# Optimization experiments

Measured on AMD Instinct MI355X. Metric: run time of the kernel, lower is better.

Reference implementation:

```python
import jax, jax.numpy as jnp
import numpy as np

N, D, H, E, K = 4096, 512, 2048, 8, 2  # tokens, input_size, hidden_size, num_experts, top_k


def setup_inputs() -> dict:
    key = jax.random.key(0)
    ks = jax.random.split(key, 4)
    x = jax.random.normal(ks[0], (N, D), dtype=jnp.float32)
    # torch init: weights ~ N(0, 0.001), biases zero
    Wg = jax.random.normal(ks[1], (D, E), dtype=jnp.float32) * 0.001
    bg = jnp.zeros((E,), jnp.float32)
    W1 = jax.random.normal(ks[2], (E, D, H), dtype=jnp.float32) * 0.001
    b1 = jnp.zeros((E, H), jnp.float32)
    W2 = jax.random.normal(ks[3], (E, H, D), dtype=jnp.float32) * 0.001
    b2 = jnp.zeros((E, D), jnp.float32)
    return {"x": x, "Wg": Wg, "bg": bg, "W1": W1, "b1": b1, "W2": W2, "b2": b2}


def reference(x, Wg, bg, W1, b1, W2, b2):
    # Gating: softmax over experts
    gates = jax.nn.softmax(x @ Wg + bg, axis=-1)            # [N, E]
    top_w, top_i = jax.lax.top_k(gates, K)                  # [N, K]
    top_w = top_w / jnp.sum(top_w, axis=-1, keepdims=True)  # renormalize

    # Expert MLP (fc1 -> fc2, no nonlinearity per source). Vectorized across all
    # experts, then gather the top-k selected outputs per token.
    h1 = jnp.einsum('nd,edh->neh', x, W1) + b1              # [N, E, H]
    all_out = jnp.einsum('neh,ehd->ned', h1, W2) + b2       # [N, E, D]
    sel = jnp.take_along_axis(all_out, top_i[:, :, None], axis=1)  # [N, K, D]

    combined = jnp.einsum('nkd,nk->nd', sel, top_w)         # [N, D]

    # usage counts: scatter-add of (detached) top-k weights per expert
    usage = jnp.zeros((E,), x.dtype).at[top_i.reshape(-1)].add(
        jax.lax.stop_gradient(top_w).reshape(-1))
    return combined, usage
```

## Files before the change

### kernel.cpp

```cpp
#include <hip/hip_runtime.h>
#include <hip/hip_bf16.h>


#define N_TOK 4096
#define DIM   512
#define HID   2048
#define NEXP  8
#define TOTSLOT (2 * N_TOK)
#define M1TILE 72
#define M2TILE 144

typedef __attribute__((ext_vector_type(8))) short short8;
typedef __attribute__((ext_vector_type(4))) float f32x4;

static __device__ __forceinline__ unsigned short f2bf(float f) {
    __hip_bfloat16 b = __float2bfloat16(f);
    return *reinterpret_cast<unsigned short*>(&b);
}
static __device__ __forceinline__ float bf2f(unsigned short u) {
    return __uint_as_float((unsigned)u << 16);
}

static __device__ __forceinline__ void load16_to_lds(const void* g, void* l) {
    __builtin_amdgcn_global_load_lds(
        (const __attribute__((address_space(1))) unsigned int*)g,
        (__attribute__((address_space(3))) unsigned int*)l, 16, 0, 0);
}

__global__ __launch_bounds__(256) void gating_kernel(
    const float* __restrict__ x, const float* __restrict__ Wg,
    const float* __restrict__ bg,
    int* __restrict__ cnt, int* __restrict__ te, float* __restrict__ tw,
    float* __restrict__ usage, unsigned short* __restrict__ Xb)
{
    __shared__ int   lcnt[NEXP];
    __shared__ float lus[NEXP];
    int tid = threadIdx.x;
    if (tid < NEXP) { lcnt[tid] = 0; lus[tid] = 0.f; }
    __syncthreads();

    int wave = tid >> 6;
    int lane = tid & 63;

    for (int t = 0; t < 4; ++t) {
        int n = blockIdx.x * 16 + wave * 4 + t;

        float acc[NEXP];
#pragma unroll
        for (int e = 0; e < NEXP; ++e) acc[e] = 0.f;

#pragma unroll
        for (int it = 0; it < DIM / 64; ++it) {
            int d = it * 64 + lane;
            float xv = x[n * DIM + d];
            Xb[n * DIM + d] = f2bf(xv);
            float4 wa = *(const float4*)&Wg[d * NEXP];
            float4 wb = *(const float4*)&Wg[d * NEXP + 4];
            acc[0] += xv * wa.x; acc[1] += xv * wa.y;
            acc[2] += xv * wa.z; acc[3] += xv * wa.w;
            acc[4] += xv * wb.x; acc[5] += xv * wb.y;
            acc[6] += xv * wb.z; acc[7] += xv * wb.w;
        }
#pragma unroll
        for (int m = 32; m >= 1; m >>= 1) {
#pragma unroll
            for (int e = 0; e < NEXP; ++e)
                acc[e] += __shfl_xor(acc[e], m, 64);
        }
        if (lane == 0) {
            float l[NEXP];
#pragma unroll
            for (int e = 0; e < NEXP; ++e) l[e] = acc[e] + bg[e];
            int i0 = 0;
#pragma unroll
            for (int e = 1; e < NEXP; ++e) if (l[e] > l[i0]) i0 = e;
            int i1 = (i0 == 0) ? 1 : 0;
#pragma unroll
            for (int e = 0; e < NEXP; ++e)
                if (e != i0 && l[e] > l[i1]) i1 = e;
            float w0 = 1.f / (1.f + expf(l[i1] - l[i0]));
            float w1 = 1.f - w0;
            te[n * 2] = i0; te[n * 2 + 1] = i1;
            tw[n * 2] = w0; tw[n * 2 + 1] = w1;
            atomicAdd(&lcnt[i0], 1);
            atomicAdd(&lcnt[i1], 1);
            atomicAdd(&lus[i0], w0);
            atomicAdd(&lus[i1], w1);
        }
    }
    __syncthreads();
    if (tid < NEXP) {
        if (lcnt[tid]) atomicAdd(&cnt[tid], lcnt[tid]);
        if (lus[tid] != 0.f) atomicAdd(&usage[tid], lus[tid]);
    }
}

__global__ void prefix_kernel(const int* __restrict__ cnt,
                              int* __restrict__ offs, int* __restrict__ fill,
                              int* __restrict__ tb128, int* __restrict__ tb64,
                              int* __restrict__ ntile)
{
    if (threadIdx.x == 0) {
        int s = 0, a = 0, b = 0;
        for (int e = 0; e < NEXP; ++e) {
            offs[e] = s; s += cnt[e];
            tb128[e] = a; a += (cnt[e] + 127) >> 7;
            tb64[e]  = b; b += (cnt[e] + 63) >> 6;
        }
        tb128[NEXP] = a; tb64[NEXP] = b;
        ntile[0] = a; ntile[1] = b;
    }
    if (threadIdx.x < NEXP) fill[threadIdx.x] = 0;
}

__global__ __launch_bounds__(256) void scatter_kernel(
    int* __restrict__ te, const float* __restrict__ tw,
    const int* __restrict__ offs, int* __restrict__ fill,
    int* __restrict__ btok, float* __restrict__ bwt)
{
    __shared__ int lcnt[NEXP];
    __shared__ int gbase[NEXP];
    int tid = threadIdx.x;
    if (tid < NEXP) lcnt[tid] = 0;
    __syncthreads();
    int n = blockIdx.x * 256 + tid;
    int e0 = te[n * 2], e1 = te[n * 2 + 1];
    int l0 = atomicAdd(&lcnt[e0], 1);
    int l1 = atomicAdd(&lcnt[e1], 1);
    __syncthreads();
    if (tid < NEXP) gbase[tid] = atomicAdd(&fill[tid], lcnt[tid]);
    __syncthreads();
    int s0 = offs[e0] + gbase[e0] + l0;
    int s1 = offs[e1] + gbase[e1] + l1;
    btok[s0] = n; bwt[s0] = tw[n * 2];
    btok[s1] = n; bwt[s1] = tw[n * 2 + 1];
    te[n * 2] = s0; te[n * 2 + 1] = s1;
}

__global__ __launch_bounds__(256) void transpose_cvt_kernel(
    const float* __restrict__ W1, const float* __restrict__ W2,
    unsigned short* __restrict__ W1t, unsigned short* __restrict__ W2t,
    int* __restrict__ cnt, float* __restrict__ usage)
{
    __shared__ unsigned short tile[64][65];
    int tid = threadIdx.x;
    int bx = blockIdx.x, z = blockIdx.y;
    if (bx == 0 && z == 0 && tid < NEXP) { cnt[tid] = 0; usage[tid] = 0.f; }

    const float* in; unsigned short* outp; int R, C, rt, ct, e;
    if (z < NEXP) { e = z;        in = W1; outp = W1t; R = DIM; C = HID; rt = bx >> 5; ct = bx & 31; }
    else          { e = z - NEXP; in = W2; outp = W2t; R = HID; C = DIM; rt = bx >> 3; ct = bx & 7;  }
    const float* src = in + (size_t)e * R * C;
    unsigned short* dst = outp + (size_t)e * R * C;
    int r0 = rt * 64, c0 = ct * 64;
    int rr = tid >> 2, cb = (tid & 3) * 16;
#pragma unroll
    for (int i = 0; i < 4; ++i) {
        float4 v = *(const float4*)&src[(size_t)(r0 + rr) * C + c0 + cb + i * 4];
        tile[rr][cb + i * 4 + 0] = f2bf(v.x);
        tile[rr][cb + i * 4 + 1] = f2bf(v.y);
        tile[rr][cb + i * 4 + 2] = f2bf(v.z);
        tile[rr][cb + i * 4 + 3] = f2bf(v.w);
    }
    __syncthreads();
#pragma unroll
    for (int i = 0; i < 4; ++i) {
        ushort4 u;
        u.x = tile[cb + i * 4 + 0][rr];
        u.y = tile[cb + i * 4 + 1][rr];
        u.z = tile[cb + i * 4 + 2][rr];
        u.w = tile[cb + i * 4 + 3][rr];
        *(ushort4*)&dst[(size_t)(c0 + rr) * R + r0 + cb + i * 4] = u;
    }
}


__global__ __launch_bounds__(256) void gemm1_kernel(
    const unsigned short* __restrict__ Xb, const unsigned short* __restrict__ W1t,
    const float* __restrict__ b1, const int* __restrict__ cnt,
    const int* __restrict__ offs, const int* __restrict__ btok,
    const int* __restrict__ tb128, const int* __restrict__ ntile,
    unsigned short* __restrict__ H1)
{
    __shared__ __align__(16) unsigned short Ws[2][128 * 64];
    __shared__ __align__(16) unsigned short Xs[2][128 * 64];
    __shared__ int tok_s[128];

    int bx = blockIdx.x;
    int ti = (bx & 7) * (M1TILE / 8) + (bx >> 3);
    if (ti >= ntile[0]) return;
    int e = 0;
#pragma unroll
    for (int k = 1; k < NEXP; ++k) if (ti >= tb128[k]) e = k;
    int tt = ti - tb128[e];
    int ht = blockIdx.y;
    int cn = cnt[e];
    int off_e = offs[e];
    int tid = threadIdx.x;

    if (tid < 128) {
        int lr = tt * 128 + tid;
        tok_s[tid] = (lr < cn) ? btok[off_e + lr] : 0;
    }
    __syncthreads();

    int wave = tid >> 6, lane = tid & 63;
    int mbase = (wave >> 1) * 64, nbase = (wave & 1) * 64;
    int quad = lane >> 4, lcol = lane & 15;
    f32x4 acc[4][4];
#pragma unroll
    for (int mi = 0; mi < 4; ++mi)
#pragma unroll
        for (int ni = 0; ni < 4; ++ni)
            acc[mi][ni] = (f32x4){0.f, 0.f, 0.f, 0.f};

    int Rb = tid >> 3, pc = tid & 7;
    const unsigned short* Wsrc = W1t + ((size_t)e * HID + ht * 128) * DIM;

    auto stage = [&](int buf, int k0) {
#pragma unroll
        for (int p = 0; p < 4; ++p) {
            int R = Rb + p * 32;
            int c = pc ^ (R & 7);
            load16_to_lds(&Wsrc[(size_t)R * DIM + k0 + c * 8], &Ws[buf][R * 64 + pc * 8]);
            load16_to_lds(&Xb[(size_t)tok_s[R] * DIM + k0 + c * 8], &Xs[buf][R * 64 + pc * 8]);
        }
    };

    stage(0, 0);

    const int NT = DIM / 64;
    for (int t = 0; t < NT; ++t) {
        int cur = t & 1;
        if (t + 1 < NT) {
            stage(cur ^ 1, (t + 1) * 64);
            asm volatile("s_waitcnt vmcnt(8)" ::: "memory");
        } else {
            asm volatile("s_waitcnt vmcnt(0)" ::: "memory");
        }
        __builtin_amdgcn_s_barrier();
        __builtin_amdgcn_sched_barrier(0);
#pragma unroll
        for (int h = 0; h < 2; ++h) {
            int cs = ((h * 4 + quad) ^ (lcol & 7)) * 8;
            short8 a[4], b[4];
#pragma unroll
            for (int i = 0; i < 4; ++i) {
                a[i] = *(const short8*)&Ws[cur][(mbase + i * 16 + lcol) * 64 + cs];
                b[i] = *(const short8*)&Xs[cur][(nbase + i * 16 + lcol) * 64 + cs];
            }
#pragma unroll
            for (int mi = 0; mi < 4; ++mi)
#pragma unroll
                for (int ni = 0; ni < 4; ++ni)
                    acc[mi][ni] = __builtin_amdgcn_mfma_f32_16x16x32_bf16(
                        a[mi], b[ni], acc[mi][ni], 0, 0, 0);
        }
        __builtin_amdgcn_sched_barrier(0);
        __builtin_amdgcn_s_barrier();
    }

    float4 bv[4];
#pragma unroll
    for (int mi = 0; mi < 4; ++mi)
        bv[mi] = *(const float4*)&b1[e * HID + ht * 128 + mbase + mi * 16 + quad * 4];
#pragma unroll
    for (int ni = 0; ni < 4; ++ni) {
        int tn = tt * 128 + nbase + ni * 16 + lcol;
        if (tn >= cn) continue;
        size_t srow = (size_t)(off_e + tn) * HID + ht * 128;
#pragma unroll
        for (int mi = 0; mi < 4; ++mi) {
            int hh = mbase + mi * 16 + quad * 4;
            ushort4 u;
            u.x = f2bf(acc[mi][ni][0] + bv[mi].x);
            u.y = f2bf(acc[mi][ni][1] + bv[mi].y);
            u.z = f2bf(acc[mi][ni][2] + bv[mi].z);
            u.w = f2bf(acc[mi][ni][3] + bv[mi].w);
            *(ushort4*)&H1[srow + hh] = u;
        }
    }
}

__global__ __launch_bounds__(256) void gemm2_kernel(
    const unsigned short* __restrict__ H1, const unsigned short* __restrict__ W2t,
    const float* __restrict__ b2, const int* __restrict__ cnt,
    const int* __restrict__ offs, const float* __restrict__ bwt,
    const int* __restrict__ tb64, const int* __restrict__ ntile,
    unsigned short* __restrict__ O)
{
    __shared__ __align__(16) unsigned short Ws[2][128 * 64];
    __shared__ __align__(16) unsigned short Hs[2][64 * 64];
    __shared__ float wt_s[64];

    int bx = blockIdx.x;
    int ti = (bx & 7) * (M2TILE / 8) + (bx >> 3);
    if (ti >= ntile[1]) return;
    int e = 0;
#pragma unroll
    for (int k = 1; k < NEXP; ++k) if (ti >= tb64[k]) e = k;
    int tt = ti - tb64[e];
    int dt = blockIdx.y;
    int cn = cnt[e];
    int off_e = offs[e];
    int sb = off_e + tt * 64;
    int tid = threadIdx.x;

    if (tid < 64) {
        int lr = tt * 64 + tid;
        wt_s[tid] = (lr < cn) ? bwt[off_e + lr] : 0.f;
    }

    int wave = tid >> 6, lane = tid & 63;
    int nbase = wave * 32;
    int quad = lane >> 4, lcol = lane & 15;
    f32x4 acc[4][2];
#pragma unroll
    for (int mi = 0; mi < 4; ++mi)
#pragma unroll
        for (int ni = 0; ni < 2; ++ni)
            acc[mi][ni] = (f32x4){0.f, 0.f, 0.f, 0.f};

    int Rb = tid >> 3, pc = tid & 7;
    const unsigned short* Wsrc = W2t + ((size_t)e * DIM + dt * 128) * HID;

    auto stage = [&](int buf, int k0) {
#pragma unroll
        for (int p = 0; p < 4; ++p) {
            int R = Rb + p * 32;
            int c = pc ^ (R & 7);
            load16_to_lds(&Wsrc[(size_t)R * HID + k0 + c * 8], &Ws[buf][R * 64 + pc * 8]);
        }
#pragma unroll
        for (int p = 0; p < 2; ++p) {
            int R = Rb + p * 32;
            int c = pc ^ (R & 7);
            int sr = sb + R; if (sr > TOTSLOT - 1) sr = TOTSLOT - 1;
            load16_to_lds(&H1[(size_t)sr * HID + k0 + c * 8], &Hs[buf][R * 64 + pc * 8]);
        }
    };

    stage(0, 0);

    const int NT = HID / 64;
    for (int t = 0; t < NT; ++t) {
        int cur = t & 1;
        if (t + 1 < NT) {
            stage(cur ^ 1, (t + 1) * 64);
            asm volatile("s_waitcnt vmcnt(6)" ::: "memory");
        } else {
            asm volatile("s_waitcnt vmcnt(0)" ::: "memory");
        }
        __builtin_amdgcn_s_barrier();
        __builtin_amdgcn_sched_barrier(0);
#pragma unroll
        for (int h = 0; h < 2; ++h) {
            int cs = ((h * 4 + quad) ^ (lcol & 7)) * 8;
            short8 a[4], b[2];
#pragma unroll
            for (int i = 0; i < 4; ++i)
                a[i] = *(const short8*)&Hs[cur][(i * 16 + lcol) * 64 + cs];
#pragma unroll
            for (int i = 0; i < 2; ++i)
                b[i] = *(const short8*)&Ws[cur][(nbase + i * 16 + lcol) * 64 + cs];
#pragma unroll
            for (int mi = 0; mi < 4; ++mi)
#pragma unroll
                for (int ni = 0; ni < 2; ++ni)
                    acc[mi][ni] = __builtin_amdgcn_mfma_f32_16x16x32_bf16(
                        a[mi], b[ni], acc[mi][ni], 0, 0, 0);
        }
        __builtin_amdgcn_sched_barrier(0);
        __builtin_amdgcn_s_barrier();
    }

    unsigned short* Oe = O + (size_t)sb * DIM + dt * 128;
#pragma unroll
    for (int ni = 0; ni < 2; ++ni) {
        int dl = nbase + ni * 16 + lcol;
        float bv = b2[e * DIM + dt * 128 + dl];
#pragma unroll
        for (int mi = 0; mi < 4; ++mi) {
            int rl = mi * 16 + quad * 4;
#pragma unroll
            for (int r = 0; r < 4; ++r) {
                int sl = rl + r;
                if (tt * 64 + sl < cn)
                    Oe[(size_t)sl * DIM + dl] = f2bf(wt_s[sl] * (acc[mi][ni][r] + bv));
            }
        }
    }
}

__global__ __launch_bounds__(256) void combine_kernel(
    const unsigned short* __restrict__ O, const int* __restrict__ sidx,
    float* __restrict__ out)
{
    int tid = threadIdx.x;
    int n = blockIdx.x * 2 + (tid >> 7);
    int dd = (tid & 127) * 4;
    int s0 = sidx[n * 2], s1 = sidx[n * 2 + 1];
    ushort4 a = *(const ushort4*)&O[(size_t)s0 * DIM + dd];
    ushort4 c = *(const ushort4*)&O[(size_t)s1 * DIM + dd];
    float4 o;
    o.x = bf2f(a.x) + bf2f(c.x);
    o.y = bf2f(a.y) + bf2f(c.y);
    o.z = bf2f(a.z) + bf2f(c.z);
    o.w = bf2f(a.w) + bf2f(c.w);
    *(float4*)&out[(size_t)n * DIM + dd] = o;
}

#define TN 16
#define HC 256
#define NCHUNK (HID / HC)

__global__ __launch_bounds__(256) void gating_fb_kernel(
    const float* __restrict__ x, const float* __restrict__ Wg,
    const float* __restrict__ bg,
    int* __restrict__ cnt, int* __restrict__ btok, float* __restrict__ bwt,
    float* __restrict__ usage)
{
    int wave = threadIdx.x >> 6;
    int lane = threadIdx.x & 63;
    int n = blockIdx.x * 4 + wave;
    float acc[NEXP];
#pragma unroll
    for (int e = 0; e < NEXP; ++e) acc[e] = 0.f;
    for (int d = lane; d < DIM; d += 64) {
        float xv = x[n * DIM + d];
        float4 wa = *(const float4*)&Wg[d * NEXP];
        float4 wb = *(const float4*)&Wg[d * NEXP + 4];
        acc[0] += xv * wa.x; acc[1] += xv * wa.y;
        acc[2] += xv * wa.z; acc[3] += xv * wa.w;
        acc[4] += xv * wb.x; acc[5] += xv * wb.y;
        acc[6] += xv * wb.z; acc[7] += xv * wb.w;
    }
#pragma unroll
    for (int m = 32; m >= 1; m >>= 1)
#pragma unroll
        for (int e = 0; e < NEXP; ++e)
            acc[e] += __shfl_xor(acc[e], m, 64);
    if (lane == 0) {
        float l[NEXP];
#pragma unroll
        for (int e = 0; e < NEXP; ++e) l[e] = acc[e] + bg[e];
        int i0 = 0;
#pragma unroll
        for (int e = 1; e < NEXP; ++e) if (l[e] > l[i0]) i0 = e;
        int i1 = (i0 == 0) ? 1 : 0;
#pragma unroll
        for (int e = 0; e < NEXP; ++e)
            if (e != i0 && l[e] > l[i1]) i1 = e;
        float w0 = 1.f / (1.f + expf(l[i1] - l[i0]));
        float w1 = 1.f - w0;
        int p0 = atomicAdd(&cnt[i0], 1);
        btok[i0 * N_TOK + p0] = n; bwt[i0 * N_TOK + p0] = w0;
        int p1 = atomicAdd(&cnt[i1], 1);
        btok[i1 * N_TOK + p1] = n; bwt[i1 * N_TOK + p1] = w1;
        atomicAdd(&usage[i0], w0);
        atomicAdd(&usage[i1], w1);
    }
}

__global__ __launch_bounds__(256) void expert_fb_kernel(
    const float* __restrict__ x, const float* __restrict__ W1,
    const float* __restrict__ b1, const float* __restrict__ W2,
    const float* __restrict__ b2, const int* __restrict__ cnt,
    const int* __restrict__ btok, const float* __restrict__ bwt,
    float* __restrict__ out)
{
    __shared__ float xs[TN][DIM];
    __shared__ float h1s[TN][HC];
    __shared__ int   tok_s[TN];
    __shared__ float wt_s[TN];
    int e = blockIdx.x >> 8;
    int tile = blockIdx.x & 255;
    int cn = cnt[e];
    int n0 = tile * TN;
    if (n0 >= cn) return;
    int nt = min(TN, cn - n0);
    int tid = threadIdx.x;
    if (tid < TN) {
        if (tid < nt) { tok_s[tid] = btok[e * N_TOK + n0 + tid]; wt_s[tid] = bwt[e * N_TOK + n0 + tid]; }
        else          { tok_s[tid] = 0; wt_s[tid] = 0.f; }
    }
    __syncthreads();
    for (int idx = tid; idx < TN * DIM; idx += 256) {
        int t = idx >> 9, d = idx & 511;
        xs[t][d] = (t < nt) ? x[tok_s[t] * DIM + d] : 0.f;
    }
    const float* W1e = W1 + (size_t)e * DIM * HID;
    const float* W2e = W2 + (size_t)e * HID * DIM;
    int tg = tid >> 6, lane = tid & 63;
    float oacc[4][8];
    {
        float4 ba = *(const float4*)&b2[e * DIM + lane * 8];
        float4 bb = *(const float4*)&b2[e * DIM + lane * 8 + 4];
#pragma unroll
        for (int ti = 0; ti < 4; ++ti) {
            oacc[ti][0] = ba.x; oacc[ti][1] = ba.y; oacc[ti][2] = ba.z; oacc[ti][3] = ba.w;
            oacc[ti][4] = bb.x; oacc[ti][5] = bb.y; oacc[ti][6] = bb.z; oacc[ti][7] = bb.w;
        }
    }
    __syncthreads();
    for (int ch = 0; ch < NCHUNK; ++ch) {
        int h0 = ch * HC;
        float f[4][4];
        {
            float4 b1v = *(const float4*)&b1[e * HID + h0 + lane * 4];
#pragma unroll
            for (int ti = 0; ti < 4; ++ti) {
                f[ti][0] = b1v.x; f[ti][1] = b1v.y; f[ti][2] = b1v.z; f[ti][3] = b1v.w;
            }
        }
        for (int d = 0; d < DIM; ++d) {
            float4 w1v = *(const float4*)&W1e[(size_t)d * HID + h0 + lane * 4];
#pragma unroll
            for (int ti = 0; ti < 4; ++ti) {
                float xv = xs[tg + 4 * ti][d];
                f[ti][0] += xv * w1v.x; f[ti][1] += xv * w1v.y;
                f[ti][2] += xv * w1v.z; f[ti][3] += xv * w1v.w;
            }
        }
        __syncthreads();
#pragma unroll
        for (int ti = 0; ti < 4; ++ti)
            *(float4*)&h1s[tg + 4 * ti][lane * 4] = make_float4(f[ti][0], f[ti][1], f[ti][2], f[ti][3]);
        __syncthreads();
        for (int j = 0; j < HC; ++j) {
            const float* w2row = &W2e[(size_t)(h0 + j) * DIM + lane * 8];
            float4 wa = *(const float4*)w2row;
            float4 wb = *(const float4*)(w2row + 4);
#pragma unroll
            for (int ti = 0; ti < 4; ++ti) {
                float hv = h1s[tg + 4 * ti][j];
                oacc[ti][0] += hv * wa.x; oacc[ti][1] += hv * wa.y;
                oacc[ti][2] += hv * wa.z; oacc[ti][3] += hv * wa.w;
                oacc[ti][4] += hv * wb.x; oacc[ti][5] += hv * wb.y;
                oacc[ti][6] += hv * wb.z; oacc[ti][7] += hv * wb.w;
            }
        }
    }
#pragma unroll
    for (int ti = 0; ti < 4; ++ti) {
        int t = tg + 4 * ti;
        if (t < nt) {
            float w = wt_s[t];
            float* o = &out[(size_t)tok_s[t] * DIM + lane * 8];
#pragma unroll
            for (int c = 0; c < 8; ++c)
                atomicAdd(&o[c], w * oacc[ti][c]);
        }
    }
}

extern "C" void kernel_launch(void* const* d_in, const int* in_sizes, int n_in,
                              void* d_out, int out_size, void* d_ws, size_t ws_size,
                              hipStream_t stream) {
    const float* x  = (const float*)d_in[0];
    const float* Wg = (const float*)d_in[1];
    const float* bg = (const float*)d_in[2];
    const float* W1 = (const float*)d_in[3];
    const float* b1 = (const float*)d_in[4];
    const float* W2 = (const float*)d_in[5];
    const float* b2 = (const float*)d_in[6];

    float* out   = (float*)d_out;
    float* usage = out + (size_t)N_TOK * DIM;

    char* ws = (char*)d_ws;
    int*   cnt   = (int*)(ws + 0);
    int*   fill  = (int*)(ws + 32);
    int*   offs  = (int*)(ws + 64);
    int*   tb128 = (int*)(ws + 96);
    int*   tb64  = (int*)(ws + 132);
    int*   ntile = (int*)(ws + 168);
    int*   te   = (int*)(ws + 256);
    float* tw   = (float*)(ws + 33024);
    int*   btok = (int*)(ws + 65792);
    float* bwt  = (float*)(ws + 98560);
    unsigned short* Xb  = (unsigned short*)(ws + 131328);
    unsigned short* W1t = (unsigned short*)(ws + 4325632);
    unsigned short* O   = W1t;
    unsigned short* W2t = (unsigned short*)(ws + 21102848);
    unsigned short* H1  = (unsigned short*)(ws + 37880064);
    const size_t WS_NEED = 71434496ULL;

    if (ws_size >= WS_NEED) {
        transpose_cvt_kernel<<<dim3(256, 16), 256, 0, stream>>>(W1, W2, W1t, W2t, cnt, usage);
        gating_kernel<<<N_TOK / 16, 256, 0, stream>>>(x, Wg, bg, cnt, te, tw, usage, Xb);
        prefix_kernel<<<1, 64, 0, stream>>>(cnt, offs, fill, tb128, tb64, ntile);
        scatter_kernel<<<N_TOK / 256, 256, 0, stream>>>(te, tw, offs, fill, btok, bwt);
        gemm1_kernel<<<dim3(M1TILE, HID / 128), 256, 0, stream>>>(
            Xb, W1t, b1, cnt, offs, btok, tb128, ntile, H1);
        gemm2_kernel<<<dim3(M2TILE, DIM / 128), 256, 0, stream>>>(
            H1, W2t, b2, cnt, offs, bwt, tb64, ntile, O);
        combine_kernel<<<N_TOK / 2, 256, 0, stream>>>(O, te, out);
    } else {
        int*   fcnt  = (int*)d_ws;
        int*   fbtok = (int*)((char*)d_ws + 256);
        float* fbwt  = (float*)((char*)d_ws + 256 + (size_t)NEXP * N_TOK * sizeof(int));
        hipMemsetAsync(d_out, 0, (size_t)(N_TOK * DIM + NEXP) * sizeof(float), stream);
        hipMemsetAsync(d_ws, 0, 256, stream);
        gating_fb_kernel<<<N_TOK / 4, 256, 0, stream>>>(x, Wg, bg, fcnt, fbtok, fbwt, usage);
        expert_fb_kernel<<<NEXP * (N_TOK / TN), 256, 0, stream>>>(
            x, W1, b1, W2, b2, fcnt, fbtok, fbwt, out);
    }
}
```

Baseline: 208.1 us.

## Fuse weight transpose with gating and fold prefix scan into scatter

The weight transpose/convert kernel and the gating kernel are merged into one launch, with blocks dispatched by block index. Gating now writes per-block expert counts and usage partials instead of using global atomics. The scatter kernel recomputes the prefix sums from those partials, which drops the separate prefix kernel and the global fill atomics. This removes two kernel launches and the serial dependencies between them, at the cost of each scatter block redundantly scanning 256x8 partial counts.

Measured after the change: 209.8 us. About the same (+0.8%).

```diff
diff --git a/kernel.cpp b/kernel.cpp
--- a/kernel.cpp
+++ b/kernel.cpp
@@ -9,6 +9,7 @@
 #define TOTSLOT (2 * N_TOK)
 #define M1TILE 72
 #define M2TILE 144
+#define NGATE  256
 
 typedef __attribute__((ext_vector_type(8))) short short8;
 typedef __attribute__((ext_vector_type(4))) float f32x4;
@@ -27,15 +28,52 @@
         (__attribute__((address_space(3))) unsigned int*)l, 16, 0, 0);
 }
 
-__global__ __launch_bounds__(256) void gating_kernel(
+__global__ __launch_bounds__(256) void prep_kernel(
+    const float* __restrict__ W1, const float* __restrict__ W2,
+    unsigned short* __restrict__ W1t, unsigned short* __restrict__ W2t,
     const float* __restrict__ x, const float* __restrict__ Wg,
     const float* __restrict__ bg,
-    int* __restrict__ cnt, int* __restrict__ te, float* __restrict__ tw,
-    float* __restrict__ usage, unsigned short* __restrict__ Xb)
+    int* __restrict__ te, float* __restrict__ tw,
+    int* __restrict__ pcnt, float* __restrict__ pus,
+    unsigned short* __restrict__ Xb)
 {
+    int bid = blockIdx.x;
+    int tid = threadIdx.x;
+
+    if (bid < 4096) {
+        __shared__ unsigned short tile[64][65];
+        int z = bid >> 8, bx = bid & 255;
+        const float* in; unsigned short* outp; int R, C, rt, ct, e;
+        if (z < NEXP) { e = z;        in = W1; outp = W1t; R = DIM; C = HID; rt = bx >> 5; ct = bx & 31; }
+        else          { e = z - NEXP; in = W2; outp = W2t; R = HID; C = DIM; rt = bx >> 3; ct = bx & 7;  }
+        const float* src = in + (size_t)e * R * C;
+        unsigned short* dst = outp + (size_t)e * R * C;
+        int r0 = rt * 64, c0 = ct * 64;
+        int rr = tid >> 2, cb = (tid & 3) * 16;
+#pragma unroll
+        for (int i = 0; i < 4; ++i) {
+            float4 v = *(const float4*)&src[(size_t)(r0 + rr) * C + c0 + cb + i * 4];
+            tile[rr][cb + i * 4 + 0] = f2bf(v.x);
+            tile[rr][cb + i * 4 + 1] = f2bf(v.y);
+            tile[rr][cb + i * 4 + 2] = f2bf(v.z);
+            tile[rr][cb + i * 4 + 3] = f2bf(v.w);
+        }
+        __syncthreads();
+#pragma unroll
+        for (int i = 0; i < 4; ++i) {
+            ushort4 u;
+            u.x = tile[cb + i * 4 + 0][rr];
+            u.y = tile[cb + i * 4 + 1][rr];
+            u.z = tile[cb + i * 4 + 2][rr];
+            u.w = tile[cb + i * 4 + 3][rr];
+            *(ushort4*)&dst[(size_t)(c0 + rr) * R + r0 + cb + i * 4] = u;
+        }
+        return;
+    }
+
     __shared__ int   lcnt[NEXP];
     __shared__ float lus[NEXP];
-    int tid = threadIdx.x;
+    int g = bid - 4096;
     if (tid < NEXP) { lcnt[tid] = 0; lus[tid] = 0.f; }
     __syncthreads();
 
@@ -43,7 +81,7 @@
     int lane = tid & 63;
 
     for (int t = 0; t < 4; ++t) {
-        int n = blockIdx.x * 16 + wave * 4 + t;
+        int n = g * 16 + wave * 4 + t;
 
         float acc[NEXP];
 #pragma unroll
@@ -90,88 +128,77 @@
     }
     __syncthreads();
     if (tid < NEXP) {
-        if (lcnt[tid]) atomicAdd(&cnt[tid], lcnt[tid]);
-        if (lus[tid] != 0.f) atomicAdd(&usage[tid], lus[tid]);
-    }
-}
-
-__global__ void prefix_kernel(const int* __restrict__ cnt,
-                              int* __restrict__ offs, int* __restrict__ fill,
-                              int* __restrict__ tb128, int* __restrict__ tb64,
-                              int* __restrict__ ntile)
-{
-    if (threadIdx.x == 0) {
-        int s = 0, a = 0, b = 0;
-        for (int e = 0; e < NEXP; ++e) {
-            offs[e] = s; s += cnt[e];
-            tb128[e] = a; a += (cnt[e] + 127) >> 7;
-            tb64[e]  = b; b += (cnt[e] + 63) >> 6;
-        }
-        tb128[NEXP] = a; tb64[NEXP] = b;
-        ntile[0] = a; ntile[1] = b;
-    }
-    if (threadIdx.x < NEXP) fill[threadIdx.x] = 0;
+        pcnt[g * NEXP + tid] = lcnt[tid];
+        pus[g * NEXP + tid]  = lus[tid];
+    }
 }
 
 __global__ __launch_bounds__(256) void scatter_kernel(
     int* __restrict__ te, const float* __restrict__ tw,
-    const int* __restrict__ offs, int* __restrict__ fill,
-    int* __restrict__ btok, float* __restrict__ bwt)
+    const int* __restrict__ pcnt, const float* __restrict__ pus,
+    int* __restrict__ btok, float* __restrict__ bwt,
+    int* __restrict__ cnt, int* __restrict__ offs,
+    int* __restrict__ tb128, int* __restrict__ tb64, int* __restrict__ ntile,
+    float* __restrict__ usage)
 {
-    __shared__ int lcnt[NEXP];
-    __shared__ int gbase[NEXP];
-    int tid = threadIdx.x;
-    if (tid < NEXP) lcnt[tid] = 0;
-    __syncthreads();
-    int n = blockIdx.x * 256 + tid;
+    __shared__ int pc[NGATE * NEXP];
+    __shared__ int cnt_s[NEXP], off_s[NEXP], base_s[NEXP], lrank[NEXP];
+    int tid = threadIdx.x, b = blockIdx.x;
+
+    {
+        const int4* src = (const int4*)pcnt;
+        int4* dst = (int4*)pc;
+        dst[tid]       = src[tid];
+        dst[tid + 256] = src[tid + 256];
+    }
+    if (tid < NEXP) lrank[tid] = 0;
+    __syncthreads();
+
+    if (tid < NEXP) {
+        int e = tid, s = 0, pre = 0;
+        for (int g = 0; g < NGATE; ++g) {
+            int v = pc[g * NEXP + e];
+            if (g < b * 16) pre += v;
+            s += v;
+        }
+        cnt_s[e] = s; base_s[e] = pre;
+    }
+    __syncthreads();
+    if (tid == 0) {
+        int o = 0;
+        for (int e = 0; e < NEXP; ++e) { off_s[e] = o; o += cnt_s[e]; }
+    }
+    __syncthreads();
+    if (tid < NEXP) base_s[tid] += off_s[tid];
+
+    if (b == 0) {
+        if (tid < NEXP) {
+            cnt[tid] = cnt_s[tid]; offs[tid] = off_s[tid];
+            float s = 0.f;
+            for (int g = 0; g < NGATE; ++g) s += pus[g * NEXP + tid];
+            usage[tid] = s;
+        }
+        if (tid == 0) {
+            int a = 0, bb = 0;
+            for (int e = 0; e < NEXP; ++e) {
+                tb128[e] = a; a += (cnt_s[e] + 127) >> 7;
+                tb64[e]  = bb; bb += (cnt_s[e] + 63) >> 6;
+            }
+            tb128[NEXP] = a; tb64[NEXP] = bb;
+            ntile[0] = a; ntile[1] = bb;
+        }
+    }
+    __syncthreads();
+
+    int n = b * 256 + tid;
     int e0 = te[n * 2], e1 = te[n * 2 + 1];
-    int l0 = atomicAdd(&lcnt[e0], 1);
-    int l1 = atomicAdd(&lcnt[e1], 1);
-    __syncthreads();
-    if (tid < NEXP) gbase[tid] = atomicAdd(&fill[tid], lcnt[tid]);
-    __syncthreads();
-    int s0 = offs[e0] + gbase[e0] + l0;
-    int s1 = offs[e1] + gbase[e1] + l1;
+    int l0 = atomicAdd(&lrank[e0], 1);
+    int l1 = atomicAdd(&lrank[e1], 1);
+    int s0 = base_s[e0] + l0;
+    int s1 = base_s[e1] + l1;
     btok[s0] = n; bwt[s0] = tw[n * 2];
     btok[s1] = n; bwt[s1] = tw[n * 2 + 1];
     te[n * 2] = s0; te[n * 2 + 1] = s1;
-}
-
-__global__ __launch_bounds__(256) void transpose_cvt_kernel(
-    const float* __restrict__ W1, const float* __restrict__ W2,
-    unsigned short* __restrict__ W1t, unsigned short* __restrict__ W2t,
-    int* __restrict__ cnt, float* __restrict__ usage)
-{
-    __shared__ unsigned short tile[64][65];
-    int tid = threadIdx.x;
-    int bx = blockIdx.x, z = blockIdx.y;
-    if (bx == 0 && z == 0 && tid < NEXP) { cnt[tid] = 0; usage[tid] = 0.f; }
-
-    const float* in; unsigned short* outp; int R, C, rt, ct, e;
-    if (z < NEXP) { e = z;        in = W1; outp = W1t; R = DIM; C = HID; rt = bx >> 5; ct = bx & 31; }
-    else          { e = z - NEXP; in = W2; outp = W2t; R = HID; C = DIM; rt = bx >> 3; ct = bx & 7;  }
-    const float* src = in + (size_t)e * R * C;
-    unsigned short* dst = outp + (size_t)e * R * C;
-    int r0 = rt * 64, c0 = ct * 64;
-    int rr = tid >> 2, cb = (tid & 3) * 16;
-#pragma unroll
-    for (int i = 0; i < 4; ++i) {
-        float4 v = *(const float4*)&src[(size_t)(r0 + rr) * C + c0 + cb + i * 4];
-        tile[rr][cb + i * 4 + 0] = f2bf(v.x);
-        tile[rr][cb + i * 4 + 1] = f2bf(v.y);
-        tile[rr][cb + i * 4 + 2] = f2bf(v.z);
-        tile[rr][cb + i * 4 + 3] = f2bf(v.w);
-    }
-    __syncthreads();
-#pragma unroll
-    for (int i = 0; i < 4; ++i) {
-        ushort4 u;
-        u.x = tile[cb + i * 4 + 0][rr];
-        u.y = tile[cb + i * 4 + 1][rr];
-        u.z = tile[cb + i * 4 + 2][rr];
-        u.w = tile[cb + i * 4 + 3][rr];
-        *(ushort4*)&dst[(size_t)(c0 + rr) * R + r0 + cb + i * 4] = u;
-    }
 }
 
 
@@ -570,27 +597,28 @@
 
     char* ws = (char*)d_ws;
     int*   cnt   = (int*)(ws + 0);
-    int*   fill  = (int*)(ws + 32);
     int*   offs  = (int*)(ws + 64);
-    int*   tb128 = (int*)(ws + 96);
-    int*   tb64  = (int*)(ws + 132);
-    int*   ntile = (int*)(ws + 168);
-    int*   te   = (int*)(ws + 256);
-    float* tw   = (float*)(ws + 33024);
-    int*   btok = (int*)(ws + 65792);
-    float* bwt  = (float*)(ws + 98560);
-    unsigned short* Xb  = (unsigned short*)(ws + 131328);
-    unsigned short* W1t = (unsigned short*)(ws + 4325632);
+    int*   tb128 = (int*)(ws + 128);
+    int*   tb64  = (int*)(ws + 192);
+    int*   ntile = (int*)(ws + 256);
+    int*   pcnt  = (int*)(ws + 512);
+    float* pus   = (float*)(ws + 8704);
+    int*   te    = (int*)(ws + 16896);
+    float* tw    = (float*)(ws + 49664);
+    int*   btok  = (int*)(ws + 82432);
+    float* bwt   = (float*)(ws + 115200);
+    unsigned short* Xb  = (unsigned short*)(ws + 147968);
+    unsigned short* W1t = (unsigned short*)(ws + 4342272);
     unsigned short* O   = W1t;
-    unsigned short* W2t = (unsigned short*)(ws + 21102848);
-    unsigned short* H1  = (unsigned short*)(ws + 37880064);
-    const size_t WS_NEED = 71434496ULL;
+    unsigned short* W2t = (unsigned short*)(ws + 21119488);
+    unsigned short* H1  = (unsigned short*)(ws + 37896704);
+    const size_t WS_NEED = 71451136ULL;
 
     if (ws_size >= WS_NEED) {
-        transpose_cvt_kernel<<<dim3(256, 16), 256, 0, stream>>>(W1, W2, W1t, W2t, cnt, usage);
-        gating_kernel<<<N_TOK / 16, 256, 0, stream>>>(x, Wg, bg, cnt, te, tw, usage, Xb);
-        prefix_kernel<<<1, 64, 0, stream>>>(cnt, offs, fill, tb128, tb64, ntile);
-        scatter_kernel<<<N_TOK / 256, 256, 0, stream>>>(te, tw, offs, fill, btok, bwt);
+        prep_kernel<<<4096 + NGATE, 256, 0, stream>>>(
+            W1, W2, W1t, W2t, x, Wg, bg, te, tw, pcnt, pus, Xb);
+        scatter_kernel<<<N_TOK / 256, 256, 0, stream>>>(
+            te, tw, pcnt, pus, btok, bwt, cnt, offs, tb128, tb64, ntile, usage);
         gemm1_kernel<<<dim3(M1TILE, HID / 128), 256, 0, stream>>>(
             Xb, W1t, b1, cnt, offs, btok, tb128, ntile, H1);
         gemm2_kernel<<<dim3(M2TILE, DIM / 128), 256, 0, stream>>>(
```
